# Performance work log

Measured on AMD Instinct MI355X. Metric: run time of the kernel, lower is better.

The kernel has to match this reference:

```python
import jax, jax.numpy as jnp
import numpy as np

A_BITS = 3
W_BITS = 3

def setup_inputs() -> dict:
    key = jax.random.key(0)
    k1, k2 = jax.random.split(key)
    # activations: small nonnegative ints (will be clipped to [0, 2^A_bits-1])
    x = jax.random.randint(k1, (32, 256, 56, 56), 0, 2 ** A_BITS, dtype=jnp.int32)
    # weights: torch.randint(0, 2**W_bits - 1, ...) -> values in [0, 6]
    weight = jax.random.randint(k2, (256, 256, 3, 3), 0, 2 ** W_BITS - 1).astype(jnp.float32)
    return {"x": x, "weight": weight}

def reference(x, weight):
    # quantize: clip activations to [0, 2^A_bits - 1]; truncate weight to int
    xq = jnp.clip(x.astype(jnp.int32), 0, 2 ** A_BITS - 1).astype(jnp.float32)
    wq = weight.astype(jnp.int32).astype(jnp.float32)  # OIHW, nonneg small ints
    # direct conv2d, stride 1, no padding (VALID). Small ints -> exact in fp32.
    out = jax.lax.conv_general_dilated(
        xq, wq,
        window_strides=(1, 1),
        padding="VALID",
        dimension_numbers=("NCHW", "OIHW", "NCHW"),
    )
    return out  # [32, 256, 54, 54]
```

## Files before the change

### kernel.cpp

```cpp
#include <hip/hip_runtime.h>
#include <stdint.h>

typedef int i32x4 __attribute__((ext_vector_type(4)));
typedef float f32x4 __attribute__((ext_vector_type(4)));

#define N_IMG 32
#define C_IN 256
#define H_IN 56
#define W_IN 56
#define K_OUT 256
#define H_OUT 54
#define W_OUT 54
#define HW_OUT 2916
#define M_PIX 93312
#define CHW_OUT 746496

#define BM 192
#define NSTEP 18

#define XT_BYTES ((size_t)N_IMG * H_IN * W_IN * C_IN)
#define WT_BYTES ((size_t)9 * K_OUT * C_IN)

#define A_OFF1 24576
#define B_OFF0 49152
#define B_STRIDE 32768

__global__ __launch_bounds__(256) void xform(const int* __restrict__ x,
                                             const float* __restrict__ w,
                                             unsigned char* __restrict__ xt,
                                             unsigned char* __restrict__ wt) {
    const int bid = blockIdx.x;
    if (bid < N_IMG * H_IN) {
        const int n = bid / H_IN;
        const int h = bid % H_IN;
        const int c = threadIdx.x;
        const int* src = x + ((size_t)((n * C_IN + c) * H_IN + h)) * W_IN;
        unsigned char* dst = xt + ((size_t)(n * H_IN + h) * W_IN) * C_IN + c;
        #pragma unroll
        for (int w0 = 0; w0 < W_IN; w0 += 4) {
            int4 v = *(const int4*)(src + w0);
            int a[4] = {v.x, v.y, v.z, v.w};
            #pragma unroll
            for (int j = 0; j < 4; ++j) {
                int q = a[j] < 0 ? 0 : (a[j] > 7 ? 7 : a[j]);
                dst[(size_t)(w0 + j) * C_IN] = (unsigned char)q;
            }
        }
    } else {
        const int k = bid - N_IMG * H_IN;
        const int c = threadIdx.x;
        const float* src = w + ((size_t)k * C_IN + c) * 9;
        #pragma unroll
        for (int rs = 0; rs < 9; ++rs) {
            int iv = (int)src[rs];
            wt[((size_t)rs * K_OUT + k) * C_IN + c] = (unsigned char)iv;
        }
    }
}

__device__ __forceinline__ void gload_lds16(const void* g, void* l) {
    __builtin_amdgcn_global_load_lds(
        (const __attribute__((address_space(1))) uint32_t*)g,
        (__attribute__((address_space(3))) uint32_t*)l,
        16, 0, 0);
}

__device__ __forceinline__ unsigned lds_off(const void* p) {
    return (unsigned)(unsigned long long)(__attribute__((address_space(3))) const char*)p;
}

#define DSREAD(dst, addr) \
    asm volatile("ds_read_b128 %0, %1" : "=v"(dst) : "v"(addr))

__global__ __launch_bounds__(512, 2) void conv_mfma(const unsigned char* __restrict__ xt,
                                                    const unsigned char* __restrict__ wt,
                                                    float* __restrict__ out) {
    __shared__ __align__(16) unsigned char lds[114688];

    const int t512 = threadIdx.x;
    const int l    = t512 & 63;
    const int wid  = t512 >> 6;
    const int wr   = wid >> 2;
    const int wc   = wid & 3;
    const int mb   = blockIdx.x;

    const int srow = t512 >> 3;
    const int cs   = (((t512 & 7) ^ (srow & 7)) << 4);
    const int tb16 = t512 * 16;

    int abase[3], bbase[4];
    #pragma unroll
    for (int i = 0; i < 3; ++i) {
        const int m   = mb * BM + i * 64 + srow;
        const int n   = m / HW_OUT;
        const int rem = m - n * HW_OUT;
        const int ho  = rem / W_OUT;
        const int wo  = rem - ho * W_OUT;
        abase[i] = (((n * H_IN + ho) * W_IN + wo) << 8) + cs;
    }
    #pragma unroll
    for (int j = 0; j < 4; ++j)
        bbase[j] = ((j * 64 + srow) << 8) + cs;

    const int lrow = l & 15;
    const int lk   = (l >> 4) << 4;
    const unsigned swz = (unsigned)((lrow & 7) << 4);
    const unsigned colk[2] = { ((unsigned)lk) ^ swz, ((unsigned)(64 + lk)) ^ swz };
    unsigned arow128[6], brow128[4];
    #pragma unroll
    for (int mf = 0; mf < 6; ++mf) arow128[mf] = (unsigned)((wr * 96 + mf * 16 + lrow) << 7);
    #pragma unroll
    for (int nf = 0; nf < 4; ++nf) brow128[nf] = (unsigned)((wc * 64 + nf * 16 + lrow) << 7);

    i32x4 acc[6][4];
    #pragma unroll
    for (int i = 0; i < 6; ++i)
        #pragma unroll
        for (int j = 0; j < 4; ++j)
            acc[i][j] = (i32x4){0, 0, 0, 0};

    const char* xb = (const char*)xt;
    const char* wb = (const char*)wt;
    const unsigned ldsb = lds_off(lds);

    #define STAGE(T, SEL) do {                                              \
        const int rs_ = (T) >> 1, ch_ = ((T) & 1) << 7;                     \
        const int r_ = rs_ / 3, s_ = rs_ - r_ * 3;                          \
        const int ast_ = ((r_ * W_IN + s_) << 8) + ch_;                     \
        const int bst_ = rs_ * (K_OUT * C_IN) + ch_;                        \
        unsigned char* pa_ = lds + (SEL) * A_OFF1 + tb16;                   \
        unsigned char* pb_ = lds + B_OFF0 + (SEL) * B_STRIDE + tb16;        \
        gload_lds16(xb + abase[0] + ast_, pa_);                             \
        gload_lds16(xb + abase[1] + ast_, pa_ + 8192);                      \
        gload_lds16(xb + abase[2] + ast_, pa_ + 16384);                     \
        gload_lds16(wb + bbase[0] + bst_, pb_);                             \
        gload_lds16(wb + bbase[1] + bst_, pb_ + 8192);                      \
        gload_lds16(wb + bbase[2] + bst_, pb_ + 16384);                     \
        gload_lds16(wb + bbase[3] + bst_, pb_ + 24576);                     \
    } while (0)

    #define KBODY(CUR, DO_STAGE, TN) do {                                   \
        const unsigned aB = ldsb + (CUR) * A_OFF1;                          \
        const unsigned bB = ldsb + B_OFF0 + (CUR) * B_STRIDE;               \
        i32x4 a0[6], b0[4], a1[6], b1[4];                                   \
        _Pragma("unroll")                                                   \
        for (int mf = 0; mf < 6; ++mf) DSREAD(a0[mf], aB + arow128[mf] + colk[0]); \
        _Pragma("unroll")                                                   \
        for (int nf = 0; nf < 4; ++nf) DSREAD(b0[nf], bB + brow128[nf] + colk[0]); \
        if (DO_STAGE) STAGE(TN, ((TN) & 1));                                \
        _Pragma("unroll")                                                   \
        for (int mf = 0; mf < 6; ++mf) DSREAD(a1[mf], aB + arow128[mf] + colk[1]); \
        _Pragma("unroll")                                                   \
        for (int nf = 0; nf < 4; ++nf) DSREAD(b1[nf], bB + brow128[nf] + colk[1]); \
        asm volatile("s_waitcnt lgkmcnt(10)" ::: "memory");                 \
        __builtin_amdgcn_sched_barrier(0);                                  \
        __builtin_amdgcn_s_setprio(1);                                      \
        _Pragma("unroll")                                                   \
        for (int mf = 0; mf < 6; ++mf)                                      \
            _Pragma("unroll")                                               \
            for (int nf = 0; nf < 4; ++nf)                                  \
                acc[mf][nf] = __builtin_amdgcn_mfma_i32_16x16x64_i8(        \
                    a0[mf], b0[nf], acc[mf][nf], 0, 0, 0);                  \
        __builtin_amdgcn_s_setprio(0);                                      \
        asm volatile("s_waitcnt lgkmcnt(0)" ::: "memory");                  \
        __builtin_amdgcn_sched_barrier(0);                                  \
        __builtin_amdgcn_s_setprio(1);                                      \
        _Pragma("unroll")                                                   \
        for (int mf = 0; mf < 6; ++mf)                                      \
            _Pragma("unroll")                                               \
            for (int nf = 0; nf < 4; ++nf)                                  \
                acc[mf][nf] = __builtin_amdgcn_mfma_i32_16x16x64_i8(        \
                    a1[mf], b1[nf], acc[mf][nf], 0, 0, 0);                  \
        __builtin_amdgcn_s_setprio(0);                                      \
    } while (0)

    STAGE(0, 0);
    asm volatile("s_waitcnt vmcnt(0)" ::: "memory");
    __builtin_amdgcn_s_barrier();

    for (int t = 0; t < NSTEP - 1; ++t) {
        KBODY((t & 1), 1, (t + 1));
        asm volatile("s_waitcnt vmcnt(0)" ::: "memory");
        __builtin_amdgcn_s_barrier();
    }
    KBODY(((NSTEP - 1) & 1), 0, 0);

    const int c16 = l & 15;
    const int p4  = (l >> 4) << 2;
    #pragma unroll
    for (int mf = 0; mf < 6; ++mf) {
        const int m   = mb * BM + wr * 96 + mf * 16 + p4;
        const int n   = m / HW_OUT;
        const int rem = m - n * HW_OUT;
        float* ob = out + (size_t)n * CHW_OUT + rem;
        #pragma unroll
        for (int nf = 0; nf < 4; ++nf) {
            const int ch = wc * 64 + nf * 16 + c16;
            f32x4 v;
            #pragma unroll
            for (int j = 0; j < 4; ++j) v[j] = (float)acc[mf][nf][j];
            *(f32x4*)(ob + (size_t)ch * HW_OUT) = v;
        }
    }
    #undef KBODY
    #undef STAGE
}

__global__ __launch_bounds__(256) void conv_naive(const int* __restrict__ x,
                                                  const float* __restrict__ w,
                                                  float* __restrict__ out) {
    int idx = blockIdx.x * 256 + threadIdx.x;
    if (idx >= N_IMG * K_OUT * HW_OUT) return;
    const int wo = idx % W_OUT;
    int tmp = idx / W_OUT;
    const int ho = tmp % H_OUT; tmp /= H_OUT;
    const int k = tmp % K_OUT;
    const int n = tmp / K_OUT;
    float acc = 0.f;
    for (int c = 0; c < C_IN; ++c) {
        const int* xp = x + ((size_t)((n * C_IN + c) * H_IN + ho)) * W_IN + wo;
        const float* wp = w + ((size_t)(k * C_IN + c)) * 9;
        #pragma unroll
        for (int r = 0; r < 3; ++r)
            #pragma unroll
            for (int s = 0; s < 3; ++s) {
                int xv = xp[r * W_IN + s];
                xv = xv < 0 ? 0 : (xv > 7 ? 7 : xv);
                acc += (float)xv * (float)(int)wp[r * 3 + s];
            }
    }
    out[idx] = acc;
}

extern "C" void kernel_launch(void* const* d_in, const int* in_sizes, int n_in,
                              void* d_out, int out_size, void* d_ws, size_t ws_size,
                              hipStream_t stream) {
    const int*   x = (const int*)d_in[0];
    const float* w = (const float*)d_in[1];
    float* out = (float*)d_out;

    const size_t need = XT_BYTES + WT_BYTES;
    if (ws_size >= need) {
        unsigned char* xt = (unsigned char*)d_ws;
        unsigned char* wt = (unsigned char*)((char*)d_ws + XT_BYTES);
        hipLaunchKernelGGL(xform, dim3(N_IMG * H_IN + K_OUT), dim3(256), 0, stream,
                           x, w, xt, wt);
        hipLaunchKernelGGL(conv_mfma, dim3(M_PIX / BM), dim3(512), 0, stream,
                           xt, wt, out);
    } else {
        const int total = N_IMG * K_OUT * HW_OUT;
        hipLaunchKernelGGL(conv_naive, dim3((total + 255) / 256), dim3(256), 0, stream, x, w, out);
    }
}
```

Measured before the change: 88.99 us.

## Stage a contiguous activation halo once per channel half and reuse across taps

Instead of reloading a fresh 192-row A tile from global memory for each of the nine filter taps, each block loads a 448-pixel contiguous halo of the channel-last input into LDS once per 128-channel half. All taps then read shifted rows from that halo. This cuts global and L2 traffic for activations by about a factor of nine. In exchange it grows LDS to 120KB, which drops occupancy from two blocks to one per CU. It also adds a serialising halo reload with an extra barrier at the channel-half boundary, and per-tap swizzle address arithmetic.

```diff
diff --git a/kernel.cpp b/kernel.cpp
--- a/kernel.cpp
+++ b/kernel.cpp
@@ -16,13 +16,12 @@
 #define CHW_OUT 746496
 
 #define BM 192
-#define NSTEP 18
 
 #define XT_BYTES ((size_t)N_IMG * H_IN * W_IN * C_IN)
 #define WT_BYTES ((size_t)9 * K_OUT * C_IN)
 
-#define A_OFF1 24576
-#define B_OFF0 49152
+#define HALO_ROWS 448
+#define B_OFF 57344
 #define B_STRIDE 32768
 
 __global__ __launch_bounds__(256) void xform(const int* __restrict__ x,
@@ -72,10 +71,10 @@
 #define DSREAD(dst, addr) \
     asm volatile("ds_read_b128 %0, %1" : "=v"(dst) : "v"(addr))
 
-__global__ __launch_bounds__(512, 2) void conv_mfma(const unsigned char* __restrict__ xt,
-                                                    const unsigned char* __restrict__ wt,
-                                                    float* __restrict__ out) {
-    __shared__ __align__(16) unsigned char lds[114688];
+__global__ __launch_bounds__(512) void conv_mfma(const unsigned char* __restrict__ xt,
+                                                 const unsigned char* __restrict__ wt,
+                                                 float* __restrict__ out) {
+    __shared__ __align__(16) unsigned char lds[122880];
 
     const int t512 = threadIdx.x;
     const int l    = t512 & 63;
@@ -88,29 +87,35 @@
     const int cs   = (((t512 & 7) ^ (srow & 7)) << 4);
     const int tb16 = t512 * 16;
 
-    int abase[3], bbase[4];
-    #pragma unroll
-    for (int i = 0; i < 3; ++i) {
-        const int m   = mb * BM + i * 64 + srow;
+    const int m0  = mb * BM;
+    const int n0  = m0 / HW_OUT;
+    const int rm0 = m0 - n0 * HW_OUT;
+    const int oh0 = rm0 / W_OUT;
+    const int ow0 = rm0 - oh0 * W_OUT;
+    const int pix0 = n0 * (H_IN * W_IN) + oh0 * W_IN + ow0;
+
+    const int lrow = l & 15;
+    int drow[6];
+    #pragma unroll
+    for (int mf = 0; mf < 6; ++mf) {
+        const int m   = m0 + wr * 96 + mf * 16 + lrow;
         const int n   = m / HW_OUT;
         const int rem = m - n * HW_OUT;
-        const int ho  = rem / W_OUT;
-        const int wo  = rem - ho * W_OUT;
-        abase[i] = (((n * H_IN + ho) * W_IN + wo) << 8) + cs;
-    }
-    #pragma unroll
-    for (int j = 0; j < 4; ++j)
-        bbase[j] = ((j * 64 + srow) << 8) + cs;
-
-    const int lrow = l & 15;
-    const int lk   = (l >> 4) << 4;
-    const unsigned swz = (unsigned)((lrow & 7) << 4);
-    const unsigned colk[2] = { ((unsigned)lk) ^ swz, ((unsigned)(64 + lk)) ^ swz };
-    unsigned arow128[6], brow128[4];
-    #pragma unroll
-    for (int mf = 0; mf < 6; ++mf) arow128[mf] = (unsigned)((wr * 96 + mf * 16 + lrow) << 7);
+        const int oh  = rem / W_OUT;
+        const int ow  = rem - oh * W_OUT;
+        drow[mf] = n * (H_IN * W_IN) + oh * W_IN + ow - pix0;
+    }
+
+    const int lk = (l >> 4) << 4;
+    const unsigned swzB = (unsigned)((lrow & 7) << 4);
+    unsigned brow128[4];
     #pragma unroll
     for (int nf = 0; nf < 4; ++nf) brow128[nf] = (unsigned)((wc * 64 + nf * 16 + lrow) << 7);
+    const unsigned colkB[2] = { ((unsigned)lk) ^ swzB, ((unsigned)(64 + lk)) ^ swzB };
+
+    int bbase[4];
+    #pragma unroll
+    for (int j = 0; j < 4; ++j) bbase[j] = ((j * 64 + srow) << 8) + cs;
 
     i32x4 acc[6][4];
     #pragma unroll
@@ -123,35 +128,51 @@
     const char* wb = (const char*)wt;
     const unsigned ldsb = lds_off(lds);
 
-    #define STAGE(T, SEL) do {                                              \
-        const int rs_ = (T) >> 1, ch_ = ((T) & 1) << 7;                     \
-        const int r_ = rs_ / 3, s_ = rs_ - r_ * 3;                          \
-        const int ast_ = ((r_ * W_IN + s_) << 8) + ch_;                     \
-        const int bst_ = rs_ * (K_OUT * C_IN) + ch_;                        \
-        unsigned char* pa_ = lds + (SEL) * A_OFF1 + tb16;                   \
-        unsigned char* pb_ = lds + B_OFF0 + (SEL) * B_STRIDE + tb16;        \
-        gload_lds16(xb + abase[0] + ast_, pa_);                             \
-        gload_lds16(xb + abase[1] + ast_, pa_ + 8192);                      \
-        gload_lds16(xb + abase[2] + ast_, pa_ + 16384);                     \
-        gload_lds16(wb + bbase[0] + bst_, pb_);                             \
-        gload_lds16(wb + bbase[1] + bst_, pb_ + 8192);                      \
-        gload_lds16(wb + bbase[2] + bst_, pb_ + 16384);                     \
-        gload_lds16(wb + bbase[3] + bst_, pb_ + 24576);                     \
+    #define STAGE_HALO(CH) do {                                             \
+        const char* hsrc_ = xb + (size_t)pix0 * 256 + (size_t)(CH) * 128;   \
+        _Pragma("unroll")                                                   \
+        for (int i_ = 0; i_ < 7; ++i_)                                      \
+            gload_lds16(hsrc_ + (size_t)(((i_ * 64 + srow) << 8) + cs),     \
+                        lds + i_ * 8192 + tb16);                            \
     } while (0)
 
-    #define KBODY(CUR, DO_STAGE, TN) do {                                   \
-        const unsigned aB = ldsb + (CUR) * A_OFF1;                          \
-        const unsigned bB = ldsb + B_OFF0 + (CUR) * B_STRIDE;               \
+    #define STAGE_B(TAP, CH, SEL) do {                                      \
+        const char* bsrc_ = wb + (size_t)(TAP) * (K_OUT * C_IN) + (size_t)(CH) * 128; \
+        unsigned char* bdst_ = lds + B_OFF + (size_t)(SEL) * B_STRIDE + tb16; \
+        gload_lds16(bsrc_ + bbase[0], bdst_);                               \
+        gload_lds16(bsrc_ + bbase[1], bdst_ + 8192);                        \
+        gload_lds16(bsrc_ + bbase[2], bdst_ + 16384);                       \
+        gload_lds16(bsrc_ + bbase[3], bdst_ + 24576);                       \
+    } while (0)
+
+    #define KBODY(G, DO_STAGE) do {                                         \
+        const int ch_  = ((G) >= 9) ? 1 : 0;                                \
+        const int tap_ = (G) - ch_ * 9;                                     \
+        const int r_   = (tap_ * 11) >> 5;                                  \
+        const int s_   = tap_ - r_ * 3;                                     \
+        const int toff_ = r_ * W_IN + s_;                                   \
+        const unsigned bB_ = ldsb + B_OFF + ((unsigned)((G) & 1)) * B_STRIDE; \
         i32x4 a0[6], b0[4], a1[6], b1[4];                                   \
-        _Pragma("unroll")                                                   \
-        for (int mf = 0; mf < 6; ++mf) DSREAD(a0[mf], aB + arow128[mf] + colk[0]); \
-        _Pragma("unroll")                                                   \
-        for (int nf = 0; nf < 4; ++nf) DSREAD(b0[nf], bB + brow128[nf] + colk[0]); \
-        if (DO_STAGE) STAGE(TN, ((TN) & 1));                                \
-        _Pragma("unroll")                                                   \
-        for (int mf = 0; mf < 6; ++mf) DSREAD(a1[mf], aB + arow128[mf] + colk[1]); \
-        _Pragma("unroll")                                                   \
-        for (int nf = 0; nf < 4; ++nf) DSREAD(b1[nf], bB + brow128[nf] + colk[1]); \
+        unsigned abase_[6], aswz_[6];                                       \
+        _Pragma("unroll")                                                   \
+        for (int mf = 0; mf < 6; ++mf) {                                    \
+            const int row_ = drow[mf] + toff_;                              \
+            abase_[mf] = ldsb + ((unsigned)row_ << 7);                      \
+            aswz_[mf]  = ((unsigned)(row_ & 7)) << 4;                       \
+            DSREAD(a0[mf], abase_[mf] + (((unsigned)lk) ^ aswz_[mf]));      \
+        }                                                                   \
+        _Pragma("unroll")                                                   \
+        for (int nf = 0; nf < 4; ++nf) DSREAD(b0[nf], bB_ + brow128[nf] + colkB[0]); \
+        if (DO_STAGE) {                                                     \
+            const int g1_ = (G) + 1;                                        \
+            const int c1_ = (g1_ >= 9) ? 1 : 0;                             \
+            STAGE_B(g1_ - c1_ * 9, c1_, (g1_ & 1));                         \
+        }                                                                   \
+        _Pragma("unroll")                                                   \
+        for (int mf = 0; mf < 6; ++mf)                                      \
+            DSREAD(a1[mf], abase_[mf] + (((unsigned)(64 + lk)) ^ aswz_[mf])); \
+        _Pragma("unroll")                                                   \
+        for (int nf = 0; nf < 4; ++nf) DSREAD(b1[nf], bB_ + brow128[nf] + colkB[1]); \
         asm volatile("s_waitcnt lgkmcnt(10)" ::: "memory");                 \
         __builtin_amdgcn_sched_barrier(0);                                  \
         __builtin_amdgcn_s_setprio(1);                                      \
@@ -174,16 +195,23 @@
         __builtin_amdgcn_s_setprio(0);                                      \
     } while (0)
 
-    STAGE(0, 0);
+    STAGE_HALO(0);
+    STAGE_B(0, 0, 0);
     asm volatile("s_waitcnt vmcnt(0)" ::: "memory");
     __builtin_amdgcn_s_barrier();
 
-    for (int t = 0; t < NSTEP - 1; ++t) {
-        KBODY((t & 1), 1, (t + 1));
-        asm volatile("s_waitcnt vmcnt(0)" ::: "memory");
-        __builtin_amdgcn_s_barrier();
-    }
-    KBODY(((NSTEP - 1) & 1), 0, 0);
+    for (int g = 0; g < 18; ++g) {
+        KBODY(g, (g < 17));
+        if (g < 17) {
+            asm volatile("s_waitcnt vmcnt(0)" ::: "memory");
+            __builtin_amdgcn_s_barrier();
+        }
+        if (g == 8) {
+            STAGE_HALO(1);
+            asm volatile("s_waitcnt vmcnt(0)" ::: "memory");
+            __builtin_amdgcn_s_barrier();
+        }
+    }
 
     const int c16 = l & 15;
     const int p4  = (l >> 4) << 2;
@@ -203,7 +231,8 @@
         }
     }
     #undef KBODY
-    #undef STAGE
+    #undef STAGE_B
+    #undef STAGE_HALO
 }
 
 __global__ __launch_bounds__(256) void conv_naive(const int* __restrict__ x,
```

Result: slower. 94.61 us (+6.3%).

## Triple-buffer LDS with 64-channel K-steps and 384x256 block tile

Applied to the files above, without the earlier changes.

Enlarges the block tile to 384 pixels by all 256 output channels, with each wave computing 96x128 and 48 accumulators. The K step shrinks to 64 channels, giving 36 steps, and a three-buffer LDS ring keeps loads two steps ahead. A and B staging are split across two MFMA half-phases and a new 4-slot XOR swizzle is used. The aim is less weight re-fetch per pixel and better overlap of global loads with MFMA. In exchange it adds barriers per step, raises register pressure from the doubled accumulators, and halves the grid size.

```diff
diff --git a/kernel.cpp b/kernel.cpp
--- a/kernel.cpp
+++ b/kernel.cpp
@@ -15,15 +15,14 @@
 #define M_PIX 93312
 #define CHW_OUT 746496
 
-#define BM 192
-#define NSTEP 18
+#define BM 384
+#define NSTEP 36
 
 #define XT_BYTES ((size_t)N_IMG * H_IN * W_IN * C_IN)
 #define WT_BYTES ((size_t)9 * K_OUT * C_IN)
 
-#define A_OFF1 24576
-#define B_OFF0 49152
-#define B_STRIDE 32768
+#define BUF_STRIDE 40960
+#define BOFF 24576
 
 __global__ __launch_bounds__(256) void xform(const int* __restrict__ x,
                                              const float* __restrict__ w,
@@ -72,118 +71,133 @@
 #define DSREAD(dst, addr) \
     asm volatile("ds_read_b128 %0, %1" : "=v"(dst) : "v"(addr))
 
+__device__ __forceinline__ int swz4(int row) { return (row ^ (row >> 2)) & 3; }
+
 __global__ __launch_bounds__(512, 2) void conv_mfma(const unsigned char* __restrict__ xt,
                                                     const unsigned char* __restrict__ wt,
                                                     float* __restrict__ out) {
-    __shared__ __align__(16) unsigned char lds[114688];
+    __shared__ __align__(16) unsigned char lds[3 * BUF_STRIDE];
 
     const int t512 = threadIdx.x;
     const int l    = t512 & 63;
     const int wid  = t512 >> 6;
-    const int wr   = wid >> 2;
-    const int wc   = wid & 3;
+    const int wr   = wid >> 1;
+    const int wc   = wid & 1;
     const int mb   = blockIdx.x;
 
-    const int srow = t512 >> 3;
-    const int cs   = (((t512 & 7) ^ (srow & 7)) << 4);
+    const int slot = t512 & 3;
+    const int trow = t512 >> 2;
     const int tb16 = t512 * 16;
 
-    int abase[3], bbase[4];
-    #pragma unroll
-    for (int i = 0; i < 3; ++i) {
-        const int m   = mb * BM + i * 64 + srow;
+    int srcA[3];
+    #pragma unroll
+    for (int rnd = 0; rnd < 3; ++rnd) {
+        const int r   = rnd * 128 + trow;
+        const int m   = mb * BM + r;
         const int n   = m / HW_OUT;
         const int rem = m - n * HW_OUT;
-        const int ho  = rem / W_OUT;
-        const int wo  = rem - ho * W_OUT;
-        abase[i] = (((n * H_IN + ho) * W_IN + wo) << 8) + cs;
-    }
-    #pragma unroll
-    for (int j = 0; j < 4; ++j)
-        bbase[j] = ((j * 64 + srow) << 8) + cs;
+        const int oh  = rem / W_OUT;
+        const int ow  = rem - oh * W_OUT;
+        srcA[rnd] = ((n * H_IN + oh) * W_IN + ow) * 256 + ((slot ^ swz4(r)) << 4);
+    }
+    int srcB[2];
+    #pragma unroll
+    for (int rnd = 0; rnd < 2; ++rnd) {
+        const int k = rnd * 128 + trow;
+        srcB[rnd] = k * 256 + ((slot ^ swz4(k)) << 4);
+    }
 
     const int lrow = l & 15;
-    const int lk   = (l >> 4) << 4;
-    const unsigned swz = (unsigned)((lrow & 7) << 4);
-    const unsigned colk[2] = { ((unsigned)lk) ^ swz, ((unsigned)(64 + lk)) ^ swz };
-    unsigned arow128[6], brow128[4];
-    #pragma unroll
-    for (int mf = 0; mf < 6; ++mf) arow128[mf] = (unsigned)((wr * 96 + mf * 16 + lrow) << 7);
-    #pragma unroll
-    for (int nf = 0; nf < 4; ++nf) brow128[nf] = (unsigned)((wc * 64 + nf * 16 + lrow) << 7);
-
-    i32x4 acc[6][4];
+    const int g    = l >> 4;
+    unsigned aoff[6], boff[8];
+    #pragma unroll
+    for (int mf = 0; mf < 6; ++mf) {
+        const int r = wr * 96 + mf * 16 + lrow;
+        aoff[mf] = (unsigned)(r * 64 + ((g ^ swz4(r)) << 4));
+    }
+    #pragma unroll
+    for (int nf = 0; nf < 8; ++nf) {
+        const int k = wc * 128 + nf * 16 + lrow;
+        boff[nf] = (unsigned)(BOFF + k * 64 + ((g ^ swz4(k)) << 4));
+    }
+
+    i32x4 acc[6][8];
     #pragma unroll
     for (int i = 0; i < 6; ++i)
         #pragma unroll
-        for (int j = 0; j < 4; ++j)
+        for (int j = 0; j < 8; ++j)
             acc[i][j] = (i32x4){0, 0, 0, 0};
 
     const char* xb = (const char*)xt;
     const char* wb = (const char*)wt;
     const unsigned ldsb = lds_off(lds);
 
-    #define STAGE(T, SEL) do {                                              \
-        const int rs_ = (T) >> 1, ch_ = ((T) & 1) << 7;                     \
-        const int r_ = rs_ / 3, s_ = rs_ - r_ * 3;                          \
-        const int ast_ = ((r_ * W_IN + s_) << 8) + ch_;                     \
-        const int bst_ = rs_ * (K_OUT * C_IN) + ch_;                        \
-        unsigned char* pa_ = lds + (SEL) * A_OFF1 + tb16;                   \
-        unsigned char* pb_ = lds + B_OFF0 + (SEL) * B_STRIDE + tb16;        \
-        gload_lds16(xb + abase[0] + ast_, pa_);                             \
-        gload_lds16(xb + abase[1] + ast_, pa_ + 8192);                      \
-        gload_lds16(xb + abase[2] + ast_, pa_ + 16384);                     \
-        gload_lds16(wb + bbase[0] + bst_, pb_);                             \
-        gload_lds16(wb + bbase[1] + bst_, pb_ + 8192);                      \
-        gload_lds16(wb + bbase[2] + bst_, pb_ + 16384);                     \
-        gload_lds16(wb + bbase[3] + bst_, pb_ + 24576);                     \
+    #define STAGE_A3(T, BUFO) do {                                          \
+        const int tap_ = (T) >> 2, cq_ = (T) & 3;                           \
+        const int r_ = tap_ / 3, s_ = tap_ - r_ * 3;                        \
+        const int ast_ = (r_ * W_IN + s_) * 256 + cq_ * 64;                 \
+        gload_lds16(xb + srcA[0] + ast_, lds + (BUFO) + tb16);              \
+        gload_lds16(xb + srcA[1] + ast_, lds + (BUFO) + 8192 + tb16);       \
+        gload_lds16(xb + srcA[2] + ast_, lds + (BUFO) + 16384 + tb16);      \
     } while (0)
-
-    #define KBODY(CUR, DO_STAGE, TN) do {                                   \
-        const unsigned aB = ldsb + (CUR) * A_OFF1;                          \
-        const unsigned bB = ldsb + B_OFF0 + (CUR) * B_STRIDE;               \
-        i32x4 a0[6], b0[4], a1[6], b1[4];                                   \
-        _Pragma("unroll")                                                   \
-        for (int mf = 0; mf < 6; ++mf) DSREAD(a0[mf], aB + arow128[mf] + colk[0]); \
-        _Pragma("unroll")                                                   \
-        for (int nf = 0; nf < 4; ++nf) DSREAD(b0[nf], bB + brow128[nf] + colk[0]); \
-        if (DO_STAGE) STAGE(TN, ((TN) & 1));                                \
-        _Pragma("unroll")                                                   \
-        for (int mf = 0; mf < 6; ++mf) DSREAD(a1[mf], aB + arow128[mf] + colk[1]); \
-        _Pragma("unroll")                                                   \
-        for (int nf = 0; nf < 4; ++nf) DSREAD(b1[nf], bB + brow128[nf] + colk[1]); \
-        asm volatile("s_waitcnt lgkmcnt(10)" ::: "memory");                 \
-        __builtin_amdgcn_sched_barrier(0);                                  \
-        __builtin_amdgcn_s_setprio(1);                                      \
-        _Pragma("unroll")                                                   \
-        for (int mf = 0; mf < 6; ++mf)                                      \
-            _Pragma("unroll")                                               \
-            for (int nf = 0; nf < 4; ++nf)                                  \
-                acc[mf][nf] = __builtin_amdgcn_mfma_i32_16x16x64_i8(        \
-                    a0[mf], b0[nf], acc[mf][nf], 0, 0, 0);                  \
-        __builtin_amdgcn_s_setprio(0);                                      \
-        asm volatile("s_waitcnt lgkmcnt(0)" ::: "memory");                  \
-        __builtin_amdgcn_sched_barrier(0);                                  \
-        __builtin_amdgcn_s_setprio(1);                                      \
-        _Pragma("unroll")                                                   \
-        for (int mf = 0; mf < 6; ++mf)                                      \
-            _Pragma("unroll")                                               \
-            for (int nf = 0; nf < 4; ++nf)                                  \
-                acc[mf][nf] = __builtin_amdgcn_mfma_i32_16x16x64_i8(        \
-                    a1[mf], b1[nf], acc[mf][nf], 0, 0, 0);                  \
-        __builtin_amdgcn_s_setprio(0);                                      \
+    #define STAGE_B2(T, BUFO) do {                                          \
+        const int tap_ = (T) >> 2, cq_ = (T) & 3;                           \
+        const int bst_ = tap_ * (K_OUT * C_IN) + cq_ * 64;                  \
+        gload_lds16(wb + srcB[0] + bst_, lds + (BUFO) + BOFF + tb16);       \
+        gload_lds16(wb + srcB[1] + bst_, lds + (BUFO) + BOFF + 8192 + tb16);\
     } while (0)
 
-    STAGE(0, 0);
+    STAGE_A3(0, 0);          STAGE_B2(0, 0);
+    STAGE_A3(1, BUF_STRIDE); STAGE_B2(1, BUF_STRIDE);
+    asm volatile("s_waitcnt vmcnt(5)" ::: "memory");
+    __builtin_amdgcn_s_barrier();
+
+    unsigned curO = 0, nxtO = BUF_STRIDE, stgO = 2 * BUF_STRIDE;
+
+    for (int t = 0; t < NSTEP; ++t) {
+        int t2 = t + 2; if (t2 >= NSTEP) t2 -= NSTEP;
+        const unsigned aB = ldsb + curO;
+        i32x4 a[6], bA[4], bB[4];
+
+        #pragma unroll
+        for (int mf = 0; mf < 6; ++mf) DSREAD(a[mf], aB + aoff[mf]);
+        #pragma unroll
+        for (int nf = 0; nf < 4; ++nf) DSREAD(bA[nf], aB + boff[nf]);
+        STAGE_A3(t2, stgO);
+        __builtin_amdgcn_s_barrier();
+        asm volatile("s_waitcnt lgkmcnt(0)" ::: "memory");
+        __builtin_amdgcn_sched_barrier(0);
+        __builtin_amdgcn_s_setprio(1);
+        #pragma unroll
+        for (int mf = 0; mf < 6; ++mf)
+            #pragma unroll
+            for (int nf = 0; nf < 4; ++nf)
+                acc[mf][nf] = __builtin_amdgcn_mfma_i32_16x16x64_i8(
+                    a[mf], bA[nf], acc[mf][nf], 0, 0, 0);
+        __builtin_amdgcn_s_setprio(0);
+        __builtin_amdgcn_s_barrier();
+
+        #pragma unroll
+        for (int nf = 0; nf < 4; ++nf) DSREAD(bB[nf], aB + boff[nf + 4]);
+        STAGE_B2(t2, stgO);
+        __builtin_amdgcn_s_barrier();
+        asm volatile("s_waitcnt lgkmcnt(0)" ::: "memory");
+        __builtin_amdgcn_sched_barrier(0);
+        __builtin_amdgcn_s_setprio(1);
+        #pragma unroll
+        for (int mf = 0; mf < 6; ++mf)
+            #pragma unroll
+            for (int nf = 0; nf < 4; ++nf)
+                acc[mf][nf + 4] = __builtin_amdgcn_mfma_i32_16x16x64_i8(
+                    a[mf], bB[nf], acc[mf][nf + 4], 0, 0, 0);
+        __builtin_amdgcn_s_setprio(0);
+        asm volatile("s_waitcnt vmcnt(5)" ::: "memory");
+        __builtin_amdgcn_s_barrier();
+
+        const unsigned tmp = curO; curO = nxtO; nxtO = stgO; stgO = tmp;
+    }
+
     asm volatile("s_waitcnt vmcnt(0)" ::: "memory");
-    __builtin_amdgcn_s_barrier();
-
-    for (int t = 0; t < NSTEP - 1; ++t) {
-        KBODY((t & 1), 1, (t + 1));
-        asm volatile("s_waitcnt vmcnt(0)" ::: "memory");
-        __builtin_amdgcn_s_barrier();
-    }
-    KBODY(((NSTEP - 1) & 1), 0, 0);
 
     const int c16 = l & 15;
     const int p4  = (l >> 4) << 2;
@@ -194,16 +208,16 @@
         const int rem = m - n * HW_OUT;
         float* ob = out + (size_t)n * CHW_OUT + rem;
         #pragma unroll
-        for (int nf = 0; nf < 4; ++nf) {
-            const int ch = wc * 64 + nf * 16 + c16;
+        for (int nf = 0; nf < 8; ++nf) {
+            const int ch = wc * 128 + nf * 16 + c16;
             f32x4 v;
             #pragma unroll
             for (int j = 0; j < 4; ++j) v[j] = (float)acc[mf][nf][j];
             *(f32x4*)(ob + (size_t)ch * HW_OUT) = v;
         }
     }
-    #undef KBODY
-    #undef STAGE
+    #undef STAGE_A3
+    #undef STAGE_B2
 }
 
 __global__ __launch_bounds__(256) void conv_naive(const int* __restrict__ x,
```

Result: slower. 102.2 us (+14.9%).
